# Kernel tuning notes

Measured on AMD Instinct MI355X. Metric: run time of the kernel, lower is better.

The kernel has to match this reference:

```python
import jax, jax.numpy as jnp
import numpy as np

HID = 2048   # hidden_size
H = 16       # num_attention_heads
D = 128      # head_dim
BLOCK = 256  # lightning attention chunk size
N = 8192     # num tokens (prefill)
EPS = 1e-5
THETA = 600000.0
NUM_LAYERS = 20
LAYER_ID = 0


def _slopes(n):
    # BailingMoELinearAttention._build_slope_tensor for power-of-2 n
    start = 2.0 ** (-2.0 ** (-(np.log2(n) - 3)))
    s = np.array([start * start ** i for i in range(n)], dtype=np.float32)
    # layer decay scaling: slope * (1 - layer_id/(L-1) + 1e-5)
    return s * (1.0 - LAYER_ID / (NUM_LAYERS - 1) + 1e-5)


def setup_inputs() -> dict:
    key = jax.random.key(0)
    ks = jax.random.split(key, 5)
    sc = 1.0 / np.sqrt(HID)
    return {
        "hidden_states": jax.random.normal(ks[0], (N, HID), jnp.float32),
        "positions": jnp.arange(N, dtype=jnp.int32),
        "Wqkv": jax.random.normal(ks[1], (HID, 3 * H * D), jnp.float32) * sc,
        "Wg": jax.random.normal(ks[2], (HID, H * D), jnp.float32) * sc,
        "Wd": jax.random.normal(ks[3], (H * D, HID), jnp.float32) * sc,
        "g_norm_weight": jnp.ones((H * D,), jnp.float32),
    }


def _rope(x, cos, sin):
    # x: [N,H,D]; neox style rotate-halves, fp32 rope
    x1, x2 = x[..., : D // 2], x[..., D // 2:]
    c, s = cos[:, None, :], sin[:, None, :]
    return jnp.concatenate([x1 * c - x2 * s, x2 * c + x1 * s], axis=-1)


def _lightning_attn(q, k, v, slopes):
    # minimax chunked linear attention with per-head exponential decay.
    # q,k,v: [H,N,D] fp32; slopes: [H]
    s = slopes[:, None, None]                                   # [H,1,1]
    arr = jnp.arange(1, BLOCK + 1, dtype=jnp.float32)           # 1..m
    q_decay = jnp.exp(-s * arr[None, :, None])                  # [H,m,1]
    k_decay = jnp.exp(-s * (BLOCK - arr)[None, :, None])        # [H,m,1]
    idx = arr[:, None] - arr[None, :]                           # [m,m]
    diag_decay = jnp.where(idx >= 0, jnp.exp(-s * idx[None]), 0.0)  # [H,m,m]
    blk_decay = jnp.exp(-slopes * BLOCK)[:, None, None]         # [H,1,1]

    NC = N // BLOCK
    qc = q.reshape(H, NC, BLOCK, D).transpose(1, 0, 2, 3)       # [NC,H,m,D]
    kc = k.reshape(H, NC, BLOCK, D).transpose(1, 0, 2, 3)
    vc = v.reshape(H, NC, BLOCK, D).transpose(1, 0, 2, 3)

    def step(kv, blk):
        qi, ki, vi = blk                                        # [H,m,D]
        o_inter = jnp.einsum('hmd,hde->hme', qi * q_decay, kv)  # cross-chunk state
        qk = jnp.einsum('hmd,hnd->hmn', qi, ki) * diag_decay    # intra-chunk causal+decay
        o_intra = jnp.einsum('hmn,hne->hme', qk, vi)
        kv = blk_decay * kv + jnp.einsum('hmd,hme->hde', ki * k_decay, vi)
        return kv, o_inter + o_intra

    kv0 = jnp.zeros((H, D, D), jnp.float32)
    _, out = jax.lax.scan(step, kv0, (qc, kc, vc))              # [NC,H,m,D]
    return out.transpose(0, 2, 1, 3).reshape(N, H * D)


def reference(hidden_states, positions, Wqkv, Wg, Wd, g_norm_weight):
    qkv = (hidden_states @ Wqkv).astype(jnp.float32)            # [N,3*H*D]
    q, k, v = jnp.split(qkv, 3, axis=-1)
    q = q.reshape(N, H, D)
    k = k.reshape(N, H, D)
    v = v.reshape(N, H, D)

    inv_freq = 1.0 / (THETA ** (jnp.arange(0, D, 2, dtype=jnp.float32) / D))
    freqs = positions.astype(jnp.float32)[:, None] * inv_freq   # [N,D/2]
    cos, sin = jnp.cos(freqs), jnp.sin(freqs)
    q = _rope(q, cos, sin)
    k = _rope(k, cos, sin)
    q = q * (D ** -0.5)                                         # linear_scale (minimax)

    slopes = jnp.asarray(_slopes(H))
    attn = _lightning_attn(q.transpose(1, 0, 2), k.transpose(1, 0, 2),
                           v.transpose(1, 0, 2), slopes)        # [N,H*D]

    # gated group RMSNorm (group_norm_size=1 -> full width), sigmoid gate, norm before gate
    gate = hidden_states @ Wg
    rms = jax.lax.rsqrt(jnp.mean(attn * attn, axis=-1, keepdims=True) + EPS)
    y = attn * rms * g_norm_weight * jax.nn.sigmoid(gate)
    return y @ Wd                                               # out projection [N,HID]
```

## Files before the change

### kernel.cpp

```cpp
#include <hip/hip_runtime.h>
#include <stdint.h>

typedef short v8s __attribute__((ext_vector_type(8)));
typedef short v4s __attribute__((ext_vector_type(4)));
typedef float v4f __attribute__((ext_vector_type(4)));

#define NTOK 8192
#define HIDD 2048
#define NH 16
#define HD 128
#define CHUNK 256
#define NCH 32
#define NQKV 6144

__device__ __forceinline__ float bf2f(short s){
  return __uint_as_float(((unsigned)(unsigned short)s) << 16);
}
__device__ __forceinline__ short f2bf(float f){
  unsigned u = __float_as_uint(f);
  unsigned r = (u + 0x7fffu + ((u >> 16) & 1u)) >> 16;
  return (short)r;
}
__device__ __forceinline__ float slope_of(int h){
  return exp2f(-0.5f * (float)(h + 1)) * 1.00001f;
}

__device__ __forceinline__ void gload_lds16(const void* g, void* l){
  __builtin_amdgcn_global_load_lds(
      (__attribute__((address_space(1))) void*)(g),
      (__attribute__((address_space(3))) void*)(l),
      16, 0, 0);
}

__global__ void rope_table_k(const int* __restrict__ pos, float* __restrict__ tab){
  int n = blockIdx.x;
  int i = threadIdx.x;
  float p = (float)pos[n];
  float ex = (float)i * (1.0f / 64.0f);
  float invf = expf(-ex * logf(600000.0f));
  float fr = p * invf;
  tab[n * 128 + i] = cosf(fr);
  tab[n * 128 + 64 + i] = sinf(fr);
}

__global__ void cvt_k(const float* __restrict__ in, short* __restrict__ outp, int n4){
  int i = blockIdx.x * 256 + threadIdx.x;
  if(i >= n4) return;
  v4f x = *(const v4f*)(in + (long)i * 4);
  v4s y;
#pragma unroll
  for(int j = 0; j < 4; j++) y[j] = f2bf(x[j]);
  *(v4s*)(outp + (long)i * 4) = y;
}

__global__ void tconv_k(const float* __restrict__ in, short* __restrict__ outp, int R, int C){
  __shared__ float tl[32][33];
  int c0 = blockIdx.x * 32, r0 = blockIdx.y * 32;
  int tx = threadIdx.x & 31, ty = threadIdx.x >> 5;
#pragma unroll
  for(int ii = 0; ii < 4; ii++){
    int r = ty + ii * 8;
    tl[r][tx] = in[(long)(r0 + r) * C + c0 + tx];
  }
  __syncthreads();
#pragma unroll
  for(int ii = 0; ii < 4; ii++){
    int r = ty + ii * 8;
    outp[(long)(c0 + r) * R + r0 + tx] = f2bf(tl[tx][r]);
  }
}

template<int EPI>
__global__ __launch_bounds__(256)
void gemm_bt_k(const short* __restrict__ A, const short* __restrict__ Bt,
               float* __restrict__ FO, short* __restrict__ SO,
               int M, int Nn, int K)
{
  __shared__ __align__(16) short sA[2][128 * 32];
  __shared__ __align__(16) short sB[2][128 * 32];
  const int t = threadIdx.x;
  const int lane = t & 63;
  const int w = t >> 6;
  const int wm = w >> 1, wn = w & 1;
  const int m0 = blockIdx.y * 128, n0 = blockIdx.x * 128;

  auto stage = [&](int buf, int k0){
#pragma unroll
    for(int j = 0; j < 2; j++){
      int L = j * 256 + t;
      int row = L >> 2;
      int co = (L & 3) << 3;
      short* lb_a = &sA[buf][(j * 256 + w * 64) * 8];
      short* lb_b = &sB[buf][(j * 256 + w * 64) * 8];
      gload_lds16(A + (long)(m0 + row) * K + k0 + co, lb_a);
      gload_lds16(Bt + (long)(n0 + row) * K + k0 + co, lb_b);
    }
  };

  v4f acc[4][4];
#pragma unroll
  for(int i = 0; i < 4; i++)
#pragma unroll
    for(int j = 0; j < 4; j++) acc[i][j] = (v4f){0.f, 0.f, 0.f, 0.f};

  const int nk = K >> 5;
  stage(0, 0);
  for(int kt = 0; kt < nk; ++kt){
    __syncthreads();
    const int cur = kt & 1;
    if(kt + 1 < nk) stage(cur ^ 1, (kt + 1) << 5);
    const int lrow = lane & 15;
    const int kofs = (lane >> 4) << 3;
    v8s af[4], bfr[4];
#pragma unroll
    for(int mi = 0; mi < 4; mi++) af[mi] = *(const v8s*)&sA[cur][(wm * 64 + mi * 16 + lrow) * 32 + kofs];
#pragma unroll
    for(int ni = 0; ni < 4; ni++) bfr[ni] = *(const v8s*)&sB[cur][(wn * 64 + ni * 16 + lrow) * 32 + kofs];
#pragma unroll
    for(int mi = 0; mi < 4; mi++)
#pragma unroll
      for(int ni = 0; ni < 4; ni++)
        acc[mi][ni] = __builtin_amdgcn_mfma_f32_16x16x32_bf16(af[mi], bfr[ni], acc[mi][ni], 0, 0, 0);
  }

  const int crow = (lane >> 4) << 2;
  const int ccol = lane & 15;
#pragma unroll
  for(int mi = 0; mi < 4; mi++){
#pragma unroll
    for(int ni = 0; ni < 4; ni++){
#pragma unroll
      for(int r = 0; r < 4; r++){
        int gr = m0 + wm * 64 + mi * 16 + crow + r;
        int gc = n0 + wn * 64 + ni * 16 + ccol;
        float vv = acc[mi][ni][r];
        if(EPI == 0){
          FO[(long)gr * Nn + gc] = vv;
        } else if(EPI == 1){
          int role = gc >> 11, hh = (gc >> 7) & 15, dd = gc & 127;
          SO[(((long)role * NH + hh) * NTOK + gr) * HD + dd] = f2bf(vv);
        } else {
          SO[(long)gr * Nn + gc] = f2bf(1.0f / (1.0f + expf(-vv)));
        }
      }
    }
  }
}

__global__ void rope_k(short* __restrict__ qkv, const float* __restrict__ tab){
  long idx = (long)blockIdx.x * 256 + threadIdx.x;
  int i8 = (int)(idx & 7);
  long rest = idx >> 3;
  int n = (int)(rest & 8191); rest >>= 13;
  int h = (int)(rest & 15);
  int role = (int)(rest >> 4);
  int i0 = i8 * 8;
  long base = (((long)role * NH + h) * NTOK + n) * HD;
  v8s x1 = *(const v8s*)(qkv + base + i0);
  v8s x2 = *(const v8s*)(qkv + base + 64 + i0);
  v4f c0 = *(const v4f*)(tab + n * 128 + i0);
  v4f c1 = *(const v4f*)(tab + n * 128 + i0 + 4);
  v4f s0 = *(const v4f*)(tab + n * 128 + 64 + i0);
  v4f s1 = *(const v4f*)(tab + n * 128 + 64 + i0 + 4);
  float sc = (role == 0) ? 0.08838834764831845f : 1.0f;
  v8s o1, o2;
#pragma unroll
  for(int j = 0; j < 4; j++){
    float a = bf2f(x1[j]), b = bf2f(x2[j]);
    o1[j] = f2bf((a * c0[j] - b * s0[j]) * sc);
    o2[j] = f2bf((b * c0[j] + a * s0[j]) * sc);
  }
#pragma unroll
  for(int j = 0; j < 4; j++){
    float a = bf2f(x1[4 + j]), b = bf2f(x2[4 + j]);
    o1[4 + j] = f2bf((a * c1[j] - b * s1[j]) * sc);
    o2[4 + j] = f2bf((b * c1[j] + a * s1[j]) * sc);
  }
  *(v8s*)(qkv + base + i0) = o1;
  *(v8s*)(qkv + base + 64 + i0) = o2;
}

__global__ __launch_bounds__(256)
void skernel(const short* __restrict__ qkv, float* __restrict__ Sb){
  int c = blockIdx.x, h = blockIdx.y;
  float s = slope_of(h);
  __shared__ __align__(16) short kT[128][40];
  __shared__ __align__(16) short vT[128][40];
  const int t = threadIdx.x, lane = t & 63, w = t >> 6;
  const int wm = w >> 1, wn = w & 1;
  const short* kb = qkv + (((long)NH + h) * NTOK + c * CHUNK) * HD;
  const short* vb = qkv + (((long)2 * NH + h) * NTOK + c * CHUNK) * HD;
  v4f acc[4][4];
#pragma unroll
  for(int i = 0; i < 4; i++)
#pragma unroll
    for(int j = 0; j < 4; j++) acc[i][j] = (v4f){0.f, 0.f, 0.f, 0.f};

  for(int n0 = 0; n0 < CHUNK; n0 += 32){
    __syncthreads();
#pragma unroll
    for(int rep = 0; rep < 2; rep++){
      int L = rep * 256 + t;
      int nn = L >> 4, d0 = (L & 15) << 3;
      v8s kx = *(const v8s*)(kb + (long)(n0 + nn) * HD + d0);
      v8s vx = *(const v8s*)(vb + (long)(n0 + nn) * HD + d0);
      float kd = expf(-s * (float)(255 - (n0 + nn)));
#pragma unroll
      for(int j = 0; j < 8; j++){
        kT[d0 + j][nn] = f2bf(bf2f(kx[j]) * kd);
        vT[d0 + j][nn] = vx[j];
      }
    }
    __syncthreads();
    const int lrow = lane & 15, kofs = (lane >> 4) << 3;
    v8s af[4], bfr[4];
#pragma unroll
    for(int ei = 0; ei < 4; ei++) af[ei] = *(const v8s*)&vT[wm * 64 + ei * 16 + lrow][kofs];
#pragma unroll
    for(int di = 0; di < 4; di++) bfr[di] = *(const v8s*)&kT[wn * 64 + di * 16 + lrow][kofs];
#pragma unroll
    for(int ei = 0; ei < 4; ei++)
#pragma unroll
      for(int di = 0; di < 4; di++)
        acc[ei][di] = __builtin_amdgcn_mfma_f32_16x16x32_bf16(af[ei], bfr[di], acc[ei][di], 0, 0, 0);
  }
  float* ob = Sb + ((long)h * NCH + c) * (HD * HD);
  const int crow = (lane >> 4) << 2, ccol = lane & 15;
#pragma unroll
  for(int ei = 0; ei < 4; ei++)
#pragma unroll
    for(int di = 0; di < 4; di++)
#pragma unroll
      for(int r = 0; r < 4; r++)
        ob[(long)(wm * 64 + ei * 16 + crow + r) * HD + wn * 64 + di * 16 + ccol] = acc[ei][di][r];
}

__global__ void scan_k(const float* __restrict__ Sb, short* __restrict__ kvb){
  int idx = blockIdx.x * 256 + threadIdx.x;
  int h = idx >> 14, ed = idx & 16383;
  float bd = expf(-slope_of(h) * 256.0f);
  float a = 0.f;
  for(int c = 0; c < NCH; c++){
    long o = ((long)h * NCH + c) * 16384 + ed;
    kvb[o] = f2bf(a);
    a = bd * a + Sb[o];
  }
}

__global__ __launch_bounds__(256)
void attn_k(const short* __restrict__ qkv, const short* __restrict__ kvb,
            short* __restrict__ attnb){
  const int c = blockIdx.x, mt = blockIdx.y, h = blockIdx.z;
  const int t = threadIdx.x, lane = t & 63, w = t >> 6;
  const float s = slope_of(h);
  __shared__ __align__(16) short Kl[64 * 128];
  __shared__ __align__(16) short VT[128][72];
  const int lrow = lane & 15, kg = lane >> 4;
  const int mbase = mt * 64 + w * 16;

  const short* qb = qkv + (((long)h) * NTOK + c * CHUNK + mbase) * HD;
  v8s qf[4];
#pragma unroll
  for(int kc = 0; kc < 4; kc++)
    qf[kc] = *(const v8s*)(qb + (long)lrow * HD + kc * 32 + kg * 8);

  v4f acc[8];
#pragma unroll
  for(int ei = 0; ei < 8; ei++) acc[ei] = (v4f){0.f, 0.f, 0.f, 0.f};

  const short* kvt = kvb + ((long)h * NCH + c) * 16384;
#pragma unroll
  for(int ei = 0; ei < 8; ei++)
#pragma unroll
    for(int kc = 0; kc < 4; kc++){
      v8s bfr = *(const v8s*)(kvt + (long)(ei * 16 + lrow) * HD + kc * 32 + kg * 8);
      acc[ei] = __builtin_amdgcn_mfma_f32_16x16x32_bf16(qf[kc], bfr, acc[ei], 0, 0, 0);
    }
  float qd[4];
#pragma unroll
  for(int r = 0; r < 4; r++) qd[r] = expf(-s * (float)(mbase + kg * 4 + r + 1));
#pragma unroll
  for(int ei = 0; ei < 8; ei++)
#pragma unroll
    for(int r = 0; r < 4; r++) acc[ei][r] *= qd[r];

  const short* kbase = qkv + (((long)NH + h) * NTOK + c * CHUNK) * HD;
  const short* vbase = qkv + (((long)2 * NH + h) * NTOK + c * CHUNK) * HD;
  for(int nc = 0; nc <= mt; nc++){
    __syncthreads();
#pragma unroll
    for(int rep = 0; rep < 4; rep++){
      int L = rep * 256 + t;
      int nn = L >> 4, d0 = (L & 15) << 3;
      v8s kx = *(const v8s*)(kbase + ((long)nc * 64 + nn) * HD + d0);
      int ba = (nn << 8) + (d0 << 1); ba ^= (nn & 7) << 4;
      *(v8s*)((char*)Kl + ba) = kx;
      v8s vx = *(const v8s*)(vbase + ((long)nc * 64 + nn) * HD + d0);
#pragma unroll
      for(int j = 0; j < 8; j++) VT[d0 + j][nn] = vx[j];
    }
    __syncthreads();
    const int m_gl = mbase + lrow;
#pragma unroll
    for(int nf = 0; nf < 4; nf++){
      v4f pT = (v4f){0.f, 0.f, 0.f, 0.f};
#pragma unroll
      for(int kc = 0; kc < 4; kc++){
        int rr = nf * 16 + lrow;
        int ba = (rr << 8) + ((kc * 32 + kg * 8) << 1); ba ^= (rr & 7) << 4;
        v8s kf = *(const v8s*)((char*)Kl + ba);
        pT = __builtin_amdgcn_mfma_f32_16x16x32_bf16(kf, qf[kc], pT, 0, 0, 0);
      }
      v4s pb;
#pragma unroll
      for(int r = 0; r < 4; r++){
        int n_gl = nc * 64 + nf * 16 + kg * 4 + r;
        float f = (n_gl <= m_gl) ? expf(-s * (float)(m_gl - n_gl)) : 0.f;
        pb[r] = f2bf(pT[r] * f);
      }
#pragma unroll
      for(int ei = 0; ei < 8; ei++){
        v4s vf = *(const v4s*)&VT[ei * 16 + lrow][nf * 16 + kg * 4];
        acc[ei] = __builtin_amdgcn_mfma_f32_16x16x16bf16_1k(pb, vf, acc[ei], 0, 0, 0);
      }
    }
  }

  short* ob = attnb + (long)(c * CHUNK + mbase) * HIDD + h * HD;
#pragma unroll
  for(int ei = 0; ei < 8; ei++)
#pragma unroll
    for(int r = 0; r < 4; r++)
      ob[(long)(kg * 4 + r) * HIDD + ei * 16 + lrow] = f2bf(acc[ei][r]);
}

__global__ __launch_bounds__(256)
void rmsgate_k(const short* __restrict__ attnb, const short* __restrict__ gsig,
               const float* __restrict__ gnw, short* __restrict__ yb){
  int n = blockIdx.x, t = threadIdx.x;
  v8s x = *(const v8s*)(attnb + (long)n * HIDD + t * 8);
  float xf[8]; float ssq = 0.f;
#pragma unroll
  for(int j = 0; j < 8; j++){ xf[j] = bf2f(x[j]); ssq += xf[j] * xf[j]; }
  for(int o = 32; o > 0; o >>= 1) ssq += __shfl_down(ssq, o, 64);
  __shared__ float rl[4];
  int lane = t & 63, w = t >> 6;
  if(lane == 0) rl[w] = ssq;
  __syncthreads();
  float tot = rl[0] + rl[1] + rl[2] + rl[3];
  float rms = rsqrtf(tot * (1.0f / 2048.0f) + 1e-5f);
  v8s g = *(const v8s*)(gsig + (long)n * HIDD + t * 8);
  v4f w0 = *(const v4f*)(gnw + t * 8);
  v4f w1 = *(const v4f*)(gnw + t * 8 + 4);
  v8s y;
#pragma unroll
  for(int j = 0; j < 4; j++) y[j] = f2bf(xf[j] * rms * w0[j] * bf2f(g[j]));
#pragma unroll
  for(int j = 0; j < 4; j++) y[4 + j] = f2bf(xf[4 + j] * rms * w1[j] * bf2f(g[4 + j]));
  *(v8s*)(yb + (long)n * HIDD + t * 8) = y;
}

extern "C" void kernel_launch(void* const* d_in, const int* in_sizes, int n_in,
                              void* d_out, int out_size, void* d_ws, size_t ws_size,
                              hipStream_t stream)
{
  (void)in_sizes; (void)n_in; (void)out_size; (void)ws_size;
  const float* hidden = (const float*)d_in[0];
  const int* positions = (const int*)d_in[1];
  const float* Wqkv = (const float*)d_in[2];
  const float* Wg = (const float*)d_in[3];
  const float* Wd = (const float*)d_in[4];
  const float* gnw = (const float*)d_in[5];
  float* out = (float*)d_out;

  char* ws = (char*)d_ws;
  const size_t HBF_B = (size_t)NTOK * HIDD * 2;
  const size_t WTR_B = (size_t)NQKV * HIDD * 2;
  const size_t KVB_B = (size_t)NH * NCH * HD * HD * 2;
  short* hbf   = (short*)(ws);
  short* yb    = hbf;
  char*  wtr   = ws + HBF_B;
  short* wqkvT = (short*)(wtr);
  short* kvb   = (short*)(wtr);
  float* tab   = (float*)(wtr + KVB_B);
  short* wgT   = (short*)(wtr + KVB_B);
  short* wdT   = (short*)(wtr);
  short* qkvbf = (short*)(ws + HBF_B + WTR_B);
  float* Sb    = (float*)(d_out);
  short* attnb = (short*)(d_out);
  short* gsig  = (short*)((char*)d_out + (size_t)NTOK * HIDD * 2);

  cvt_k<<<(NTOK * HIDD / 4) / 256, 256, 0, stream>>>(hidden, hbf, NTOK * HIDD / 4);
  tconv_k<<<dim3(NQKV / 32, HIDD / 32), 256, 0, stream>>>(Wqkv, wqkvT, HIDD, NQKV);
  gemm_bt_k<1><<<dim3(NQKV / 128, NTOK / 128), 256, 0, stream>>>(hbf, wqkvT, nullptr, qkvbf, NTOK, NQKV, HIDD);

  rope_table_k<<<NTOK, 64, 0, stream>>>(positions, tab);
  rope_k<<<(2 * NH * NTOK * 8) / 256, 256, 0, stream>>>(qkvbf, tab);

  skernel<<<dim3(NCH, NH), 256, 0, stream>>>(qkvbf, Sb);
  scan_k<<<(NH * HD * HD) / 256, 256, 0, stream>>>(Sb, kvb);
  attn_k<<<dim3(NCH, 4, NH), 256, 0, stream>>>(qkvbf, kvb, attnb);

  tconv_k<<<dim3(HIDD / 32, HIDD / 32), 256, 0, stream>>>(Wg, wgT, HIDD, HIDD);
  gemm_bt_k<2><<<dim3(HIDD / 128, NTOK / 128), 256, 0, stream>>>(hbf, wgT, nullptr, gsig, NTOK, HIDD, HIDD);

  rmsgate_k<<<NTOK, 256, 0, stream>>>(attnb, gsig, gnw, yb);

  tconv_k<<<dim3(HIDD / 32, HIDD / 32), 256, 0, stream>>>(Wd, wdT, HIDD, HIDD);
  gemm_bt_k<0><<<dim3(HIDD / 128, NTOK / 128), 256, 0, stream>>>(yb, wdT, out, nullptr, NTOK, HIDD, HIDD);
}
```

Before: 782.8 us.

## Replace 128x128 GEMM with 256x256-tile 8-wave kernel with swizzled LDS and interleaved prefetch

All three projection GEMMs now use a new kernel with 256x256 output tiles, 512 threads, and a K-step of 64 split into two 32-wide halves. LDS rows use an XOR swizzle to avoid bank conflicts. Staging of the next halves is interleaved with MFMA phases using explicit vmcnt waits, barriers and setprio. The goal is more data reuse per load and better overlap of global-to-LDS copies with compute. The cost is 128 KB of LDS, high register use from 32 accumulators, and fragile hand-written wait counts.

```diff
diff --git a/kernel.cpp b/kernel.cpp
--- a/kernel.cpp
+++ b/kernel.cpp
@@ -12,6 +12,10 @@
 #define CHUNK 256
 #define NCH 32
 #define NQKV 6144
+#define KD 2048
+
+#define VMCNT(n) asm volatile("s_waitcnt vmcnt(" #n ")" ::: "memory")
+#define BARRIER() asm volatile("s_barrier" ::: "memory")
 
 __device__ __forceinline__ float bf2f(short s){
   return __uint_as_float(((unsigned)(unsigned short)s) << 16);
@@ -71,69 +75,110 @@
 }
 
 template<int EPI>
-__global__ __launch_bounds__(256)
-void gemm_bt_k(const short* __restrict__ A, const short* __restrict__ Bt,
-               float* __restrict__ FO, short* __restrict__ SO,
-               int M, int Nn, int K)
+__global__ __launch_bounds__(512, 2)
+void gemm256_k(const short* __restrict__ A, const short* __restrict__ Bt,
+               float* __restrict__ FO, short* __restrict__ SO, int Nn)
 {
-  __shared__ __align__(16) short sA[2][128 * 32];
-  __shared__ __align__(16) short sB[2][128 * 32];
+  __shared__ __align__(16) short lds[65536];
   const int t = threadIdx.x;
   const int lane = t & 63;
   const int w = t >> 6;
-  const int wm = w >> 1, wn = w & 1;
-  const int m0 = blockIdx.y * 128, n0 = blockIdx.x * 128;
-
-  auto stage = [&](int buf, int k0){
-#pragma unroll
-    for(int j = 0; j < 2; j++){
-      int L = j * 256 + t;
-      int row = L >> 2;
-      int co = (L & 3) << 3;
-      short* lb_a = &sA[buf][(j * 256 + w * 64) * 8];
-      short* lb_b = &sB[buf][(j * 256 + w * 64) * 8];
-      gload_lds16(A + (long)(m0 + row) * K + k0 + co, lb_a);
-      gload_lds16(Bt + (long)(n0 + row) * K + k0 + co, lb_b);
-    }
+  const int wm = w >> 2, wn = w & 3;
+  const int lrow = lane & 15, kg = lane >> 4;
+  const int bm = blockIdx.y * 256, bn = blockIdx.x * 256;
+  const short* Arows = A + (long)bm * KD;
+  const short* Brows = Bt + (long)bn * KD;
+  const int r0 = t >> 2;
+  const int sc0 = ((t & 3) ^ ((r0 >> 1) & 3)) << 3;
+
+  auto stage = [&](const short* rows, int mat, int buf, int ks, int kt2){
+    short* dst = &lds[mat * 32768 + buf * 16384 + ks * 8192];
+    long koff = (long)kt2 * 64 + ks * 32 + sc0;
+    gload_lds16(rows + (long)r0 * KD + koff, dst + t * 8);
+    gload_lds16(rows + (long)(r0 + 128) * KD + koff, dst + (512 + t) * 8);
   };
-
-  v4f acc[4][4];
-#pragma unroll
-  for(int i = 0; i < 4; i++)
+  auto loadA = [&](v8s* aA, int buf, int mq, int ks){
+#pragma unroll
+    for(int m = 0; m < 4; m++){
+      int row = wm * 128 + mq * 64 + m * 16 + lrow;
+      int slot = kg ^ ((row >> 1) & 3);
+      aA[m] = *(const v8s*)&lds[buf * 16384 + ks * 8192 + row * 32 + slot * 8];
+    }
+  };
+  auto loadB = [&](v8s* bb, int buf, int ks){
+#pragma unroll
+    for(int n = 0; n < 4; n++){
+      int row = wn * 64 + n * 16 + lrow;
+      int slot = kg ^ ((row >> 1) & 3);
+      bb[n] = *(const v8s*)&lds[32768 + buf * 16384 + ks * 8192 + row * 32 + slot * 8];
+    }
+  };
+
+  v4f acc[8][4];
+#pragma unroll
+  for(int i = 0; i < 8; i++)
 #pragma unroll
     for(int j = 0; j < 4; j++) acc[i][j] = (v4f){0.f, 0.f, 0.f, 0.f};
 
-  const int nk = K >> 5;
-  stage(0, 0);
+  auto mmac = [&](v8s* aA, v8s* bb, int mq){
+    __builtin_amdgcn_s_setprio(1);
+#pragma unroll
+    for(int m = 0; m < 4; m++)
+#pragma unroll
+      for(int n = 0; n < 4; n++)
+        acc[mq * 4 + m][n] = __builtin_amdgcn_mfma_f32_16x16x32_bf16(aA[m], bb[n], acc[mq * 4 + m][n], 0, 0, 0);
+    __builtin_amdgcn_s_setprio(0);
+  };
+
+  const int nk = KD / 64;
+  stage(Brows, 1, 0, 0, 0);
+  stage(Arows, 0, 0, 0, 0);
+  stage(Arows, 0, 0, 1, 0);
+  stage(Brows, 1, 0, 1, 0);
+  stage(Brows, 1, 1, 0, 1);
+  stage(Arows, 0, 1, 0, 1);
+  VMCNT(8);
+  BARRIER();
+
   for(int kt = 0; kt < nk; ++kt){
-    __syncthreads();
-    const int cur = kt & 1;
-    if(kt + 1 < nk) stage(cur ^ 1, (kt + 1) << 5);
-    const int lrow = lane & 15;
-    const int kofs = (lane >> 4) << 3;
-    v8s af[4], bfr[4];
-#pragma unroll
-    for(int mi = 0; mi < 4; mi++) af[mi] = *(const v8s*)&sA[cur][(wm * 64 + mi * 16 + lrow) * 32 + kofs];
-#pragma unroll
-    for(int ni = 0; ni < 4; ni++) bfr[ni] = *(const v8s*)&sB[cur][(wn * 64 + ni * 16 + lrow) * 32 + kofs];
-#pragma unroll
-    for(int mi = 0; mi < 4; mi++)
-#pragma unroll
-      for(int ni = 0; ni < 4; ni++)
-        acc[mi][ni] = __builtin_amdgcn_mfma_f32_16x16x32_bf16(af[mi], bfr[ni], acc[mi][ni], 0, 0, 0);
-  }
-
-  const int crow = (lane >> 4) << 2;
+    const int cur = kt & 1, nxt = cur ^ 1;
+    v8s aA[4], bb[4];
+    loadB(bb, cur, 0);
+    loadA(aA, cur, 0, 0);
+    if(kt + 1 < nk){ stage(Arows, 0, nxt, 1, kt + 1); stage(Brows, 1, nxt, 1, kt + 1); }
+    BARRIER();
+    mmac(aA, bb, 0);
+    BARRIER();
+    loadA(aA, cur, 1, 0);
+    BARRIER();
+    mmac(aA, bb, 1);
+    if(kt + 1 < nk){ VMCNT(8); } else { VMCNT(0); }
+    BARRIER();
+    loadB(bb, cur, 1);
+    loadA(aA, cur, 0, 1);
+    if(kt + 2 < nk) stage(Brows, 1, cur, 0, kt + 2);
+    BARRIER();
+    mmac(aA, bb, 0);
+    BARRIER();
+    loadA(aA, cur, 1, 1);
+    if(kt + 2 < nk) stage(Arows, 0, cur, 0, kt + 2);
+    BARRIER();
+    mmac(aA, bb, 1);
+    if(kt + 2 < nk){ VMCNT(8); } else if(kt + 1 < nk){ VMCNT(4); } else { VMCNT(0); }
+    BARRIER();
+  }
+
+  const int crow = kg << 2;
   const int ccol = lane & 15;
 #pragma unroll
-  for(int mi = 0; mi < 4; mi++){
-#pragma unroll
-    for(int ni = 0; ni < 4; ni++){
+  for(int m = 0; m < 8; m++){
+#pragma unroll
+    for(int n = 0; n < 4; n++){
 #pragma unroll
       for(int r = 0; r < 4; r++){
-        int gr = m0 + wm * 64 + mi * 16 + crow + r;
-        int gc = n0 + wn * 64 + ni * 16 + ccol;
-        float vv = acc[mi][ni][r];
+        int gr = bm + wm * 128 + m * 16 + crow + r;
+        int gc = bn + wn * 64 + n * 16 + ccol;
+        float vv = acc[m][n][r];
         if(EPI == 0){
           FO[(long)gr * Nn + gc] = vv;
         } else if(EPI == 1){
@@ -392,7 +437,7 @@
 
   cvt_k<<<(NTOK * HIDD / 4) / 256, 256, 0, stream>>>(hidden, hbf, NTOK * HIDD / 4);
   tconv_k<<<dim3(NQKV / 32, HIDD / 32), 256, 0, stream>>>(Wqkv, wqkvT, HIDD, NQKV);
-  gemm_bt_k<1><<<dim3(NQKV / 128, NTOK / 128), 256, 0, stream>>>(hbf, wqkvT, nullptr, qkvbf, NTOK, NQKV, HIDD);
+  gemm256_k<1><<<dim3(NQKV / 256, NTOK / 256), 512, 0, stream>>>(hbf, wqkvT, nullptr, qkvbf, NQKV);
 
   rope_table_k<<<NTOK, 64, 0, stream>>>(positions, tab);
   rope_k<<<(2 * NH * NTOK * 8) / 256, 256, 0, stream>>>(qkvbf, tab);
@@ -402,10 +447,10 @@
   attn_k<<<dim3(NCH, 4, NH), 256, 0, stream>>>(qkvbf, kvb, attnb);
 
   tconv_k<<<dim3(HIDD / 32, HIDD / 32), 256, 0, stream>>>(Wg, wgT, HIDD, HIDD);
-  gemm_bt_k<2><<<dim3(HIDD / 128, NTOK / 128), 256, 0, stream>>>(hbf, wgT, nullptr, gsig, NTOK, HIDD, HIDD);
+  gemm256_k<2><<<dim3(HIDD / 256, NTOK / 256), 512, 0, stream>>>(hbf, wgT, nullptr, gsig, HIDD);
 
   rmsgate_k<<<NTOK, 256, 0, stream>>>(attnb, gsig, gnw, yb);
 
   tconv_k<<<dim3(HIDD / 32, HIDD / 32), 256, 0, stream>>>(Wd, wdT, HIDD, HIDD);
-  gemm_bt_k<0><<<dim3(HIDD / 128, NTOK / 128), 256, 0, stream>>>(yb, wdT, out, nullptr, NTOK, HIDD, HIDD);
-}
+  gemm256_k<0><<<dim3(HIDD / 256, NTOK / 256), 512, 0, stream>>>(yb, wdT, out, nullptr, HIDD);
+}
```

Measured after the change: 696.1 us. -11.1%, faster.
